# Performance work log

Hardware: AMD Instinct MI355X
Metric: run time of the kernel (lower is better)

## Reference

```python
import jax, jax.numpy as jnp
import numpy as np

W_CHAMFER = (1.0, 1.0, 1.0)
W_LAPLACE = 0.5
W_MOVE = 0.1
W_EDGE = 0.1
W_NORMAL = 1.6e-4
W_CONST = 1.0
LAP_CONST = (0.2, 1.0, 1.0)
EPS = 1e-12


def _normalize(x):
    # F.normalize(x, dim=-1): x / max(||x||, eps)
    n = jnp.sqrt(jnp.sum(x * x, axis=-1, keepdims=True))
    return x / jnp.maximum(n, EPS)


def _pairwise_sq(x, y):
    # x: (B,N,3), y: (B,M,3) -> (B,N,M) squared distances, GEMM form
    x2 = jnp.sum(x * x, -1)
    y2 = jnp.sum(y * y, -1)
    xy = jnp.einsum('bnd,bmd->bnm', x, y)
    return x2[:, :, None] + y2[:, None, :] - 2.0 * xy


def _laplace_coord(pts, lap_idx):
    # pts: (B,V,3); lap_idx: (V,10) = [8 neighbor idx (-1 invalid), self, count]
    idx = lap_idx[:, :8]
    mask = idx < 0
    safe = jnp.where(mask, 0, idx)
    nbrs = pts[:, safe]                                  # (B,V,8,3)
    nbrs = jnp.where(mask[None, :, :, None], 0.0, nbrs)
    count = lap_idx[:, -1].astype(pts.dtype)
    return pts - nbrs.sum(2) / count[None, :, None]


def setup_inputs():
    key = jax.random.key(0)
    B, M = 2, 8192
    Vs = (642, 2562, 10242)
    Es = (1920, 7680, 30720)
    ks = jax.random.split(key, 3 + 4 * 3)
    inp = {}
    inp['gt_coord'] = jax.random.normal(ks[0], (B, M, 3), jnp.float32)
    inp['gt_normal'] = _normalize(jax.random.normal(ks[1], (B, M, 3), jnp.float32))
    for i, (V, E) in enumerate(zip(Vs, Es)):
        k0, k1, k2, k3 = ks[3 + 4 * i], ks[4 + 4 * i], ks[5 + 4 * i], ks[6 + 4 * i]
        inp[f'pred_coord_{i}'] = jax.random.normal(k0, (B, V, 3), jnp.float32)
        inp[f'pred_before_{i}'] = inp[f'pred_coord_{i}'] + 0.05 * jax.random.normal(k1, (B, V, 3), jnp.float32)
        inp[f'edges_{i}'] = jax.random.randint(k2, (E, 2), 0, V)
        nbr = jax.random.randint(k3, (V, 8), 0, V)
        nbr = nbr.at[:, 6:].set(-1)                      # 6 valid neighbors, 2 invalid slots
        self_idx = jnp.arange(V)[:, None]
        count = jnp.full((V, 1), 6)
        inp[f'laplace_idx_{i}'] = jnp.concatenate([nbr, self_idx, count], axis=1)
    return inp


def reference(pred_coord_0, pred_coord_1, pred_coord_2, pred_before_0, pred_before_1, pred_before_2, gt_coord, gt_normal, laplace_idx_0, laplace_idx_1, laplace_idx_2, edges_0, edges_1, edges_2):
    preds = (pred_coord_0, pred_coord_1, pred_coord_2)
    befores = (pred_before_0, pred_before_1, pred_before_2)
    laps = (laplace_idx_0, laplace_idx_1, laplace_idx_2)
    edges_all = (edges_0, edges_1, edges_2)
    chamfer_loss = 0.0
    edge_loss = 0.0
    normal_loss = 0.0
    lap_loss = 0.0
    move_loss = 0.0
    for i in range(3):
        pred, before, lap_idx, edges = preds[i], befores[i], laps[i], edges_all[i]
        # shared pairwise distance matrix for chamfer + knn (original recomputes)
        d = _pairwise_sq(pred, gt_coord)                 # (B,V,M)
        chamfer_loss = chamfer_loss + W_CHAMFER[i] * (jnp.mean(jnp.min(d, axis=1)) + jnp.mean(jnp.min(d, axis=2)))
        knn_idx = jnp.argmin(d, axis=2)                  # (B,V): nearest gt per pred pt
        e0, e1 = edges[:, 0], edges[:, 1]
        evec = _normalize(pred[:, e0] - pred[:, e1])     # (B,E,3)
        # faithful to torch: knn.idx.flatten() then index_select -> only batch-0
        # indices ever selected since edge ids < V
        sel = knn_idx.reshape(-1)[e0]
        nrm = _normalize(gt_normal[:, sel])              # (B,E,3)
        normal_loss = normal_loss + jnp.mean(jnp.abs(jnp.sum(evec * nrm, axis=2)))
        edge_loss = edge_loss + 3.0 * jnp.mean((pred[:, e0] - pred[:, e1]) ** 2)
        l1 = _laplace_coord(before, lap_idx)
        l2 = _laplace_coord(pred, lap_idx)
        lap_loss = lap_loss + LAP_CONST[i] * 3.0 * jnp.mean((l1 - l2) ** 2)
        if i > 0:
            move_loss = move_loss + LAP_CONST[i] * 3.0 * jnp.mean((before - pred) ** 2)
    loss = chamfer_loss + W_LAPLACE * lap_loss + W_MOVE * move_loss + W_EDGE * edge_loss + W_NORMAL * normal_loss
    return W_CONST * loss
```

## Files before the change

kernel.cpp:

```cpp
#include <hip/hip_runtime.h>


#define DEV __device__ __forceinline__

#define OFF_LAP  8
#define OFF_MA0  1024
#define OFF_MA1  108592
#define OFF_MB   162376
#define MINS_END 358984

DEV unsigned ford(float f) {
    unsigned u = __float_as_uint(f);
    return (u & 0x80000000u) ? ~u : (u | 0x80000000u);
}
DEV float funord(unsigned o) {
    unsigned u = (o & 0x80000000u) ? (o ^ 0x80000000u) : ~o;
    return __uint_as_float(u);
}
DEV unsigned long long umin64(unsigned long long a, unsigned long long b) { return a < b ? a : b; }

DEV float blockReduceSum256(float v) {
    #pragma unroll
    for (int o = 32; o > 0; o >>= 1) v += __shfl_down(v, o, 64);
    __shared__ float red4[4];
    int wid = threadIdx.x >> 6;
    if ((threadIdx.x & 63) == 0) red4[wid] = v;
    __syncthreads();
    return (threadIdx.x == 0) ? (red4[0] + red4[1] + red4[2] + red4[3]) : 0.0f;
}

template<bool ARGMIN>
DEV void roleA(int a, const float* p0, const float* p1, const float* p2,
               const float* gt, char* ws, char* smem)
{
    const int b = ARGMIN ? 0 : 1;
    int vtG = a >> 5, mc = a & 31;
    int vtL, V, lvlOff; const float* predL;
    if (vtG == 0)     { vtL = 0;       V = 642;   predL = p0; lvlOff = 0; }
    else if (vtG < 4) { vtL = vtG - 1; V = 2562;  predL = p1; lvlOff = 642; }
    else              { vtL = vtG - 4; V = 10242; predL = p2; lvlOff = 3204; }
    int tid = threadIdx.x, lane = tid & 63, w = tid >> 6;
    float4* SG = (float4*)smem;
    int mbase = mc << 8;
    {
        const float* gp = gt + ((size_t)(b * 8192 + mbase + tid)) * 3;
        float gx = gp[0], gy = gp[1], gz = gp[2];
        SG[tid] = make_float4(-2.f * gx, -2.f * gy, -2.f * gz,
                              fmaf(gx, gx, fmaf(gy, gy, gz * gz)));
    }
    float px[14], py[14], pz[14];
    #pragma unroll
    for (int r = 0; r < 14; r++) {
        int vr = vtL * 896 + r * 64 + lane;
        int v = vr - (vr >= V ? V : 0);
        const float* pp = predL + ((size_t)(b * V + v)) * 3;
        px[r] = pp[0]; py[r] = pp[1]; pz[r] = pp[2];
    }
    __syncthreads();
    if (ARGMIN) {
        float best[14]; int bi[14];
        #pragma unroll
        for (int r = 0; r < 14; r++) { best[r] = 3.0e38f; bi[r] = 0; }
        #pragma unroll 4
        for (int i = 0; i < 64; i++) {
            int j = (w << 6) + i;
            float4 q = SG[j];
            int cand = mbase + j;
            #pragma unroll
            for (int r = 0; r < 14; r++) {
                float d = fmaf(q.x, px[r], fmaf(q.y, py[r], fmaf(q.z, pz[r], q.w)));
                if (d < best[r]) { best[r] = d; bi[r] = cand; }
            }
        }
        __syncthreads();
        unsigned long long* RED = (unsigned long long*)smem;
        #pragma unroll
        for (int r = 0; r < 14; r++)
            RED[w * 896 + r * 64 + lane] = ((unsigned long long)ford(best[r]) << 32) | (unsigned)bi[r];
        __syncthreads();
        unsigned long long* MA0 = (unsigned long long*)(ws + OFF_MA0);
        for (int s = tid; s < 896; s += 256) {
            unsigned long long mm = umin64(umin64(RED[s], RED[s + 896]),
                                           umin64(RED[s + 1792], RED[s + 2688]));
            int vr = vtL * 896 + s; int v = vr - (vr >= V ? V : 0);
            atomicMin(&MA0[lvlOff + v], mm);
        }
    } else {
        float best[14];
        #pragma unroll
        for (int r = 0; r < 14; r++) best[r] = 3.0e38f;
        #pragma unroll 2
        for (int i = 0; i < 64; i += 2) {
            int j = (w << 6) + i;
            float4 q0 = SG[j], q1 = SG[j + 1];
            #pragma unroll
            for (int r = 0; r < 14; r++) {
                float d0 = fmaf(q0.x, px[r], fmaf(q0.y, py[r], fmaf(q0.z, pz[r], q0.w)));
                float d1 = fmaf(q1.x, px[r], fmaf(q1.y, py[r], fmaf(q1.z, pz[r], q1.w)));
                best[r] = fminf(best[r], fminf(d0, d1));
            }
        }
        __syncthreads();
        unsigned* RED = (unsigned*)smem;
        #pragma unroll
        for (int r = 0; r < 14; r++)
            RED[w * 896 + r * 64 + lane] = ford(best[r]);
        __syncthreads();
        unsigned* MA1 = (unsigned*)(ws + OFF_MA1);
        for (int s = tid; s < 896; s += 256) {
            unsigned mm = min(min(RED[s], RED[s + 896]), min(RED[s + 1792], RED[s + 2688]));
            int vr = vtL * 896 + s; int v = vr - (vr >= V ? V : 0);
            atomicMin(&MA1[lvlOff + v], mm);
        }
    }
}

DEV void roleB(int i, const float* p0, const float* p1, const float* p2,
               const float* gt, char* ws, char* smem)
{
    int c55 = i % 55; int rest = i / 55; int mt = rest & 7; int b = rest >> 3;
    int lvl, c, V; const float* predL;
    if (c55 < 3)       { lvl = 0; c = c55;      V = 642;   predL = p0; }
    else if (c55 < 14) { lvl = 1; c = c55 - 3;  V = 2562;  predL = p1; }
    else               { lvl = 2; c = c55 - 14; V = 10242; predL = p2; }
    int tid = threadIdx.x, lane = tid & 63, w = tid >> 6;
    float4* SP = (float4*)smem;
    int vbase = c << 8;
    {
        int v = vbase + tid;
        if (v < V) {
            const float* pp = predL + ((size_t)(b * V + v)) * 3;
            float x = pp[0], y = pp[1], z = pp[2];
            SP[tid] = make_float4(-2.f * x, -2.f * y, -2.f * z,
                                  fmaf(x, x, fmaf(y, y, z * z)));
        } else SP[tid] = make_float4(0.f, 0.f, 0.f, 3.0e38f);
    }
    float gx[16], gy[16], gz[16];
    #pragma unroll
    for (int r = 0; r < 16; r++) {
        int m = (mt << 10) + r * 64 + lane;
        const float* gp = gt + ((size_t)(b * 8192 + m)) * 3;
        gx[r] = gp[0]; gy[r] = gp[1]; gz[r] = gp[2];
    }
    __syncthreads();
    float best[16];
    #pragma unroll
    for (int r = 0; r < 16; r++) best[r] = 3.0e38f;
    #pragma unroll 2
    for (int i2 = 0; i2 < 64; i2 += 2) {
        int j = (w << 6) + i2;
        float4 q0 = SP[j], q1 = SP[j + 1];
        #pragma unroll
        for (int r = 0; r < 16; r++) {
            float d0 = fmaf(q0.x, gx[r], fmaf(q0.y, gy[r], fmaf(q0.z, gz[r], q0.w)));
            float d1 = fmaf(q1.x, gx[r], fmaf(q1.y, gy[r], fmaf(q1.z, gz[r], q1.w)));
            best[r] = fminf(best[r], fminf(d0, d1));
        }
    }
    __syncthreads();
    unsigned* RED = (unsigned*)smem;
    #pragma unroll
    for (int r = 0; r < 16; r++)
        RED[(w << 10) + r * 64 + lane] = ford(best[r]);
    __syncthreads();
    unsigned* MB = (unsigned*)(ws + OFF_MB);
    for (int s = tid; s < 1024; s += 256) {
        unsigned mm = min(min(RED[s], RED[s + 1024]), min(RED[s + 2048], RED[s + 3072]));
        atomicMin(&MB[(lvl << 14) + (b << 13) + (mt << 10) + s], mm);
    }
}

__global__ __launch_bounds__(256, 4) void kMega(
    const float* __restrict__ p0, const float* __restrict__ p1, const float* __restrict__ p2,
    const float* __restrict__ b0p, const float* __restrict__ b1p, const float* __restrict__ b2p,
    const int* __restrict__ l0, const int* __restrict__ l1, const int* __restrict__ l2,
    const float* __restrict__ gt, char* ws)
{
    extern __shared__ char smem[];
    int bid = blockIdx.x;
    if (bid < 128) {
        float c = 0.0f;
        int idx = bid * 256 + threadIdx.x;
        if (idx < 26892) {
            int level, V, t;
            const float *pred, *bef; const int* lap;
            if (idx < 1284)      { level = 0; V = 642;   pred = p0; bef = b0p; lap = l0; t = idx; }
            else if (idx < 6408) { level = 1; V = 2562;  pred = p1; bef = b1p; lap = l1; t = idx - 1284; }
            else                 { level = 2; V = 10242; pred = p2; bef = b2p; lap = l2; t = idx - 6408; }
            int b = t / V;
            int v = t - b * V;
            const float* P  = pred + ((size_t)b * V + v) * 3;
            const float* Bf = bef  + ((size_t)b * V + v) * 3;
            float dx = Bf[0] - P[0], dy = Bf[1] - P[1], dz = Bf[2] - P[2];
            float sx = 0.f, sy = 0.f, sz = 0.f;
            const int* L = lap + v * 10;
            #pragma unroll
            for (int j = 0; j < 8; j++) {
                int n = L[j];
                if (n >= 0) {
                    const float* Pn = pred + ((size_t)b * V + n) * 3;
                    const float* Bn = bef  + ((size_t)b * V + n) * 3;
                    sx += Bn[0] - Pn[0]; sy += Bn[1] - Pn[1]; sz += Bn[2] - Pn[2];
                }
            }
            float invc = 1.0f / (float)L[9];
            float lx = dx - sx * invc, ly = dy - sy * invc, lz = dz - sz * invc;
            float sl = fmaf(lx, lx, fmaf(ly, ly, lz * lz));
            float sm = fmaf(dx, dx, fmaf(dy, dy, dz * dz));
            float lapc = (level == 0) ? 0.2f : 1.0f;
            float iBV = 1.0f / (2.0f * (float)V);
            c = sl * (0.5f * lapc * iBV) + ((level > 0) ? sm * (0.1f * lapc * iBV) : 0.0f);
        }
        c = blockReduceSum256(c);
        if (threadIdx.x == 0) ((float*)(ws + OFF_LAP))[bid] = c;
    }
    else if (bid < 1008) roleB(bid - 128, p0, p1, p2, gt, ws, smem);
    else if (bid < 1520) roleA<true >(bid - 1008, p0, p1, p2, gt, ws, smem);
    else                 roleA<false>(bid - 1520, p0, p1, p2, gt, ws, smem);
}

__global__ __launch_bounds__(256) void kFinal(
    const float* __restrict__ p0, const float* __restrict__ p1, const float* __restrict__ p2,
    const int* __restrict__ e0p, const int* __restrict__ e1p, const int* __restrict__ e2p,
    const float* __restrict__ gt, const float* __restrict__ gtn,
    char* ws, float* __restrict__ out)
{
    int bid = blockIdx.x, tid = threadIdx.x;
    const unsigned long long* MA0 = (const unsigned long long*)(ws + OFF_MA0);
    const unsigned* MA1 = (const unsigned*)(ws + OFF_MA1);
    const unsigned* MB  = (const unsigned*)(ws + OFF_MB);
    float c = 0.0f;
    if (bid < 106) {
        int idx = bid * 256 + tid;
        if (idx < 26892) {
            int b = idx >= 13446 ? 1 : 0;
            int s = idx - (b ? 13446 : 0);
            int v, V; const float* predL; float inv;
            if (s < 642)       { v = s;        V = 642;   predL = p0; inv = 1.f / 1284.f; }
            else if (s < 3204) { v = s - 642;  V = 2562;  predL = p1; inv = 1.f / 5124.f; }
            else               { v = s - 3204; V = 10242; predL = p2; inv = 1.f / 20484.f; }
            float d = b ? funord(MA1[s]) : funord((unsigned)(MA0[s] >> 32));
            const float* pp = predL + ((size_t)(b * V + v)) * 3;
            c = (d + fmaf(pp[0], pp[0], fmaf(pp[1], pp[1], pp[2] * pp[2]))) * inv;
        }
    } else if (bid < 298) {
        int idx = (bid - 106) * 256 + tid;
        int r = idx & 16383;
        float d = funord(MB[idx]);
        const float* gp = gt + (size_t)r * 3;
        c = (d + fmaf(gp[0], gp[0], fmaf(gp[1], gp[1], gp[2] * gp[2]))) * (1.f / 16384.f);
    } else if (bid == 298) {
        if (tid < 128) c = ((const float*)(ws + OFF_LAP))[tid];
    } else {
        int idx = (bid - 299) * 256 + tid;
        int E, V, lvlOff, t;
        const float* pred; const int* edges;
        if (idx < 3840)       { E = 1920;  V = 642;   lvlOff = 0;    pred = p0; edges = e0p; t = idx; }
        else if (idx < 19200) { E = 7680;  V = 2562;  lvlOff = 642;  pred = p1; edges = e1p; t = idx - 3840; }
        else                  { E = 30720; V = 10242; lvlOff = 3204; pred = p2; edges = e2p; t = idx - 19200; }
        int b = t / E;
        int e = t % E;
        int a0 = edges[e * 2 + 0];
        int a1 = edges[e * 2 + 1];
        const float* P = pred + (size_t)b * V * 3;
        float dx = P[a0 * 3 + 0] - P[a1 * 3 + 0];
        float dy = P[a0 * 3 + 1] - P[a1 * 3 + 1];
        float dz = P[a0 * 3 + 2] - P[a1 * 3 + 2];
        float sq = fmaf(dx, dx, fmaf(dy, dy, dz * dz));
        float inv = 1.0f / fmaxf(sqrtf(sq), 1e-12f);
        int sel = (int)(unsigned)MA0[lvlOff + a0];
        const float* nr = gtn + ((size_t)b * 8192 + sel) * 3;
        float nx = nr[0], ny = nr[1], nz = nr[2];
        float invn = 1.0f / fmaxf(sqrtf(fmaf(nx, nx, fmaf(ny, ny, nz * nz))), 1e-12f);
        float dotv = fmaf(dx, nx, fmaf(dy, ny, dz * nz)) * inv * invn;
        float iBE = 1.0f / (2.0f * (float)E);
        c = sq * (0.1f * iBE) + fabsf(dotv) * (0.00016f * iBE);
    }
    c = blockReduceSum256(c);
    if (tid == 0) {
        atomicAdd((float*)ws, c);
        __threadfence();
        unsigned t = atomicAdd((unsigned*)(ws + 4), 1u);
        if (t == gridDim.x - 1) out[0] = atomicAdd((float*)ws, 0.0f);
    }
}

extern "C" void kernel_launch(void* const* d_in, const int* in_sizes, int n_in,
                              void* d_out, int out_size, void* d_ws, size_t ws_size,
                              hipStream_t stream) {
    const float *gt, *gtn, *pred[3], *bef[3];
    const int *edg[3], *lapx[3];
    if (in_sizes[0] == 49152) {
        gt  = (const float*)d_in[0];
        gtn = (const float*)d_in[1];
        for (int i = 0; i < 3; i++) {
            pred[i] = (const float*)d_in[2 + 4 * i];
            bef[i]  = (const float*)d_in[3 + 4 * i];
            edg[i]  = (const int*)  d_in[4 + 4 * i];
            lapx[i] = (const int*)  d_in[5 + 4 * i];
        }
    } else {
        for (int i = 0; i < 3; i++) pred[i] = (const float*)d_in[i];
        for (int i = 0; i < 3; i++) bef[i]  = (const float*)d_in[3 + i];
        gt  = (const float*)d_in[6];
        gtn = (const float*)d_in[7];
        for (int i = 0; i < 3; i++) lapx[i] = (const int*)d_in[8 + i];
        for (int i = 0; i < 3; i++) edg[i]  = (const int*)d_in[11 + i];
    }

    char* ws = (char*)d_ws;
    hipMemsetAsync(ws, 0, 8, stream);
    hipMemsetAsync(ws + OFF_MA0, 0xFF, MINS_END - OFF_MA0, stream);

    kMega<<<2032, 256, 28672, stream>>>(pred[0], pred[1], pred[2],
                                        bef[0], bef[1], bef[2],
                                        lapx[0], lapx[1], lapx[2], gt, ws);
    kFinal<<<614, 256, 0, stream>>>(pred[0], pred[1], pred[2],
                                    edg[0], edg[1], edg[2], gt, gtn,
                                    ws, (float*)d_out);
}
```

Baseline: 145.5 us.

## Fuse memsets and both kernels into one persistent cooperative kernel with grid syncs

Replaces two memsets plus two kernel launches with a single cooperative persistent kernel. The kernel clears the workspace, pulls work units dynamically from an atomic counter, finalizes through grid syncs, and reduces the block-level min reduction to a pairwise scheme that needs less shared memory. The aim is to remove launch and memset overhead and to raise occupancy. The cost is three grid-wide barriers, a dynamic scheduling atomic per unit, and a grid capped at 1024 persistent blocks, which may serialize the work. A fallback keeps the old two-kernel path in case the cooperative launch fails.

```diff
diff --git a/kernel.cpp b/kernel.cpp
--- a/kernel.cpp
+++ b/kernel.cpp
@@ -1,13 +1,13 @@
 #include <hip/hip_runtime.h>
+#include <hip/hip_cooperative_groups.h>
+
+namespace cg = cooperative_groups;
 
 
 #define DEV __device__ __forceinline__
-
-#define OFF_LAP  8
 #define OFF_MA0  1024
 #define OFF_MA1  108592
 #define OFF_MB   162376
-#define MINS_END 358984
 
 DEV unsigned ford(float f) {
     unsigned u = __float_as_uint(f);
@@ -26,7 +26,9 @@
     int wid = threadIdx.x >> 6;
     if ((threadIdx.x & 63) == 0) red4[wid] = v;
     __syncthreads();
-    return (threadIdx.x == 0) ? (red4[0] + red4[1] + red4[2] + red4[3]) : 0.0f;
+    float r = (threadIdx.x == 0) ? (red4[0] + red4[1] + red4[2] + red4[3]) : 0.0f;
+    __syncthreads();
+    return r;
 }
 
 template<bool ARGMIN>
@@ -72,16 +74,40 @@
                 if (d < best[r]) { best[r] = d; bi[r] = cand; }
             }
         }
-        __syncthreads();
-        unsigned long long* RED = (unsigned long long*)smem;
+        unsigned long long key[14];
         #pragma unroll
         for (int r = 0; r < 14; r++)
-            RED[w * 896 + r * 64 + lane] = ((unsigned long long)ford(best[r]) << 32) | (unsigned)bi[r];
+            key[r] = ((unsigned long long)ford(best[r]) << 32) | (unsigned)bi[r];
+        __syncthreads();
+        unsigned long long* RED0 = (unsigned long long*)smem;
+        unsigned long long* RED1 = (unsigned long long*)(smem + 7168);
+        if (w == 0) {
+            #pragma unroll
+            for (int r = 0; r < 14; r++) RED0[r * 64 + lane] = key[r];
+        }
+        if (w == 2) {
+            #pragma unroll
+            for (int r = 0; r < 14; r++) RED1[r * 64 + lane] = key[r];
+        }
+        __syncthreads();
+        if (w == 1) {
+            #pragma unroll
+            for (int r = 0; r < 14; r++) {
+                int s = r * 64 + lane;
+                RED0[s] = umin64(RED0[s], key[r]);
+            }
+        }
+        if (w == 3) {
+            #pragma unroll
+            for (int r = 0; r < 14; r++) {
+                int s = r * 64 + lane;
+                RED1[s] = umin64(RED1[s], key[r]);
+            }
+        }
         __syncthreads();
         unsigned long long* MA0 = (unsigned long long*)(ws + OFF_MA0);
         for (int s = tid; s < 896; s += 256) {
-            unsigned long long mm = umin64(umin64(RED[s], RED[s + 896]),
-                                           umin64(RED[s + 1792], RED[s + 2688]));
+            unsigned long long mm = umin64(RED0[s], RED1[s]);
             int vr = vtL * 896 + s; int v = vr - (vr >= V ? V : 0);
             atomicMin(&MA0[lvlOff + v], mm);
         }
@@ -100,15 +126,39 @@
                 best[r] = fminf(best[r], fminf(d0, d1));
             }
         }
-        __syncthreads();
-        unsigned* RED = (unsigned*)smem;
-        #pragma unroll
-        for (int r = 0; r < 14; r++)
-            RED[w * 896 + r * 64 + lane] = ford(best[r]);
+        unsigned key[14];
+        #pragma unroll
+        for (int r = 0; r < 14; r++) key[r] = ford(best[r]);
+        __syncthreads();
+        unsigned* RED0 = (unsigned*)smem;
+        unsigned* RED1 = (unsigned*)(smem + 3584);
+        if (w == 0) {
+            #pragma unroll
+            for (int r = 0; r < 14; r++) RED0[r * 64 + lane] = key[r];
+        }
+        if (w == 2) {
+            #pragma unroll
+            for (int r = 0; r < 14; r++) RED1[r * 64 + lane] = key[r];
+        }
+        __syncthreads();
+        if (w == 1) {
+            #pragma unroll
+            for (int r = 0; r < 14; r++) {
+                int s = r * 64 + lane;
+                RED0[s] = min(RED0[s], key[r]);
+            }
+        }
+        if (w == 3) {
+            #pragma unroll
+            for (int r = 0; r < 14; r++) {
+                int s = r * 64 + lane;
+                RED1[s] = min(RED1[s], key[r]);
+            }
+        }
         __syncthreads();
         unsigned* MA1 = (unsigned*)(ws + OFF_MA1);
         for (int s = tid; s < 896; s += 256) {
-            unsigned mm = min(min(RED[s], RED[s + 896]), min(RED[s + 1792], RED[s + 2688]));
+            unsigned mm = min(RED0[s], RED1[s]);
             int vr = vtL * 896 + s; int v = vr - (vr >= V ? V : 0);
             atomicMin(&MA1[lvlOff + v], mm);
         }
@@ -157,107 +207,118 @@
             best[r] = fminf(best[r], fminf(d0, d1));
         }
     }
-    __syncthreads();
-    unsigned* RED = (unsigned*)smem;
+    unsigned key[16];
     #pragma unroll
-    for (int r = 0; r < 16; r++)
-        RED[(w << 10) + r * 64 + lane] = ford(best[r]);
+    for (int r = 0; r < 16; r++) key[r] = ford(best[r]);
+    __syncthreads();
+    unsigned* RED0 = (unsigned*)smem;
+    unsigned* RED1 = (unsigned*)(smem + 4096);
+    if (w == 0) {
+        #pragma unroll
+        for (int r = 0; r < 16; r++) RED0[r * 64 + lane] = key[r];
+    }
+    if (w == 2) {
+        #pragma unroll
+        for (int r = 0; r < 16; r++) RED1[r * 64 + lane] = key[r];
+    }
+    __syncthreads();
+    if (w == 1) {
+        #pragma unroll
+        for (int r = 0; r < 16; r++) {
+            int s = r * 64 + lane;
+            RED0[s] = min(RED0[s], key[r]);
+        }
+    }
+    if (w == 3) {
+        #pragma unroll
+        for (int r = 0; r < 16; r++) {
+            int s = r * 64 + lane;
+            RED1[s] = min(RED1[s], key[r]);
+        }
+    }
     __syncthreads();
     unsigned* MB = (unsigned*)(ws + OFF_MB);
     for (int s = tid; s < 1024; s += 256) {
-        unsigned mm = min(min(RED[s], RED[s + 1024]), min(RED[s + 2048], RED[s + 3072]));
+        unsigned mm = min(RED0[s], RED1[s]);
         atomicMin(&MB[(lvl << 14) + (b << 13) + (mt << 10) + s], mm);
     }
 }
 
-__global__ __launch_bounds__(256, 4) void kMega(
-    const float* __restrict__ p0, const float* __restrict__ p1, const float* __restrict__ p2,
-    const float* __restrict__ b0p, const float* __restrict__ b1p, const float* __restrict__ b2p,
-    const int* __restrict__ l0, const int* __restrict__ l1, const int* __restrict__ l2,
-    const float* __restrict__ gt, char* ws)
-{
-    extern __shared__ char smem[];
-    int bid = blockIdx.x;
-    if (bid < 128) {
-        float c = 0.0f;
-        int idx = bid * 256 + threadIdx.x;
-        if (idx < 26892) {
-            int level, V, t;
-            const float *pred, *bef; const int* lap;
-            if (idx < 1284)      { level = 0; V = 642;   pred = p0; bef = b0p; lap = l0; t = idx; }
-            else if (idx < 6408) { level = 1; V = 2562;  pred = p1; bef = b1p; lap = l1; t = idx - 1284; }
-            else                 { level = 2; V = 10242; pred = p2; bef = b2p; lap = l2; t = idx - 6408; }
-            int b = t / V;
-            int v = t - b * V;
-            const float* P  = pred + ((size_t)b * V + v) * 3;
-            const float* Bf = bef  + ((size_t)b * V + v) * 3;
-            float dx = Bf[0] - P[0], dy = Bf[1] - P[1], dz = Bf[2] - P[2];
-            float sx = 0.f, sy = 0.f, sz = 0.f;
-            const int* L = lap + v * 10;
-            #pragma unroll
-            for (int j = 0; j < 8; j++) {
-                int n = L[j];
-                if (n >= 0) {
-                    const float* Pn = pred + ((size_t)b * V + n) * 3;
-                    const float* Bn = bef  + ((size_t)b * V + n) * 3;
-                    sx += Bn[0] - Pn[0]; sy += Bn[1] - Pn[1]; sz += Bn[2] - Pn[2];
-                }
-            }
-            float invc = 1.0f / (float)L[9];
-            float lx = dx - sx * invc, ly = dy - sy * invc, lz = dz - sz * invc;
-            float sl = fmaf(lx, lx, fmaf(ly, ly, lz * lz));
-            float sm = fmaf(dx, dx, fmaf(dy, dy, dz * dz));
-            float lapc = (level == 0) ? 0.2f : 1.0f;
-            float iBV = 1.0f / (2.0f * (float)V);
-            c = sl * (0.5f * lapc * iBV) + ((level > 0) ? sm * (0.1f * lapc * iBV) : 0.0f);
-        }
-        c = blockReduceSum256(c);
-        if (threadIdx.x == 0) ((float*)(ws + OFF_LAP))[bid] = c;
-    }
-    else if (bid < 1008) roleB(bid - 128, p0, p1, p2, gt, ws, smem);
-    else if (bid < 1520) roleA<true >(bid - 1008, p0, p1, p2, gt, ws, smem);
-    else                 roleA<false>(bid - 1520, p0, p1, p2, gt, ws, smem);
-}
-
-__global__ __launch_bounds__(256) void kFinal(
-    const float* __restrict__ p0, const float* __restrict__ p1, const float* __restrict__ p2,
-    const int* __restrict__ e0p, const int* __restrict__ e1p, const int* __restrict__ e2p,
-    const float* __restrict__ gt, const float* __restrict__ gtn,
-    char* ws, float* __restrict__ out)
-{
-    int bid = blockIdx.x, tid = threadIdx.x;
+DEV void lapUnit(int u,
+                 const float* p0, const float* p1, const float* p2,
+                 const float* b0p, const float* b1p, const float* b2p,
+                 const int* l0, const int* l1, const int* l2, char* ws)
+{
+    float c = 0.0f;
+    int idx = u * 256 + threadIdx.x;
+    if (idx < 26892) {
+        int level, V, t;
+        const float *pred, *bef; const int* lap;
+        if (idx < 1284)      { level = 0; V = 642;   pred = p0; bef = b0p; lap = l0; t = idx; }
+        else if (idx < 6408) { level = 1; V = 2562;  pred = p1; bef = b1p; lap = l1; t = idx - 1284; }
+        else                 { level = 2; V = 10242; pred = p2; bef = b2p; lap = l2; t = idx - 6408; }
+        int b = t / V;
+        int v = t - b * V;
+        const float* P  = pred + ((size_t)b * V + v) * 3;
+        const float* Bf = bef  + ((size_t)b * V + v) * 3;
+        float dx = Bf[0] - P[0], dy = Bf[1] - P[1], dz = Bf[2] - P[2];
+        float sx = 0.f, sy = 0.f, sz = 0.f;
+        const int* L = lap + v * 10;
+        #pragma unroll
+        for (int j = 0; j < 8; j++) {
+            int n = L[j];
+            if (n >= 0) {
+                const float* Pn = pred + ((size_t)b * V + n) * 3;
+                const float* Bn = bef  + ((size_t)b * V + n) * 3;
+                sx += Bn[0] - Pn[0]; sy += Bn[1] - Pn[1]; sz += Bn[2] - Pn[2];
+            }
+        }
+        float invc = 1.0f / (float)L[9];
+        float lx = dx - sx * invc, ly = dy - sy * invc, lz = dz - sz * invc;
+        float sl = fmaf(lx, lx, fmaf(ly, ly, lz * lz));
+        float sm = fmaf(dx, dx, fmaf(dy, dy, dz * dz));
+        float lapc = (level == 0) ? 0.2f : 1.0f;
+        float iBV = 1.0f / (2.0f * (float)V);
+        c = sl * (0.5f * lapc * iBV) + ((level > 0) ? sm * (0.1f * lapc * iBV) : 0.0f);
+    }
+    c = blockReduceSum256(c);
+    if (threadIdx.x == 0) atomicAdd((float*)ws, c);
+}
+
+DEV float phase2Item(int idx,
+                     const float* p0, const float* p1, const float* p2,
+                     const int* e0p, const int* e1p, const int* e2p,
+                     const float* gt, const float* gtn, char* ws)
+{
     const unsigned long long* MA0 = (const unsigned long long*)(ws + OFF_MA0);
     const unsigned* MA1 = (const unsigned*)(ws + OFF_MA1);
     const unsigned* MB  = (const unsigned*)(ws + OFF_MB);
     float c = 0.0f;
-    if (bid < 106) {
-        int idx = bid * 256 + tid;
-        if (idx < 26892) {
-            int b = idx >= 13446 ? 1 : 0;
-            int s = idx - (b ? 13446 : 0);
-            int v, V; const float* predL; float inv;
-            if (s < 642)       { v = s;        V = 642;   predL = p0; inv = 1.f / 1284.f; }
-            else if (s < 3204) { v = s - 642;  V = 2562;  predL = p1; inv = 1.f / 5124.f; }
-            else               { v = s - 3204; V = 10242; predL = p2; inv = 1.f / 20484.f; }
-            float d = b ? funord(MA1[s]) : funord((unsigned)(MA0[s] >> 32));
-            const float* pp = predL + ((size_t)(b * V + v)) * 3;
-            c = (d + fmaf(pp[0], pp[0], fmaf(pp[1], pp[1], pp[2] * pp[2]))) * inv;
-        }
-    } else if (bid < 298) {
-        int idx = (bid - 106) * 256 + tid;
-        int r = idx & 16383;
-        float d = funord(MB[idx]);
+    if (idx < 26892) {
+        int b = idx >= 13446 ? 1 : 0;
+        int s = idx - (b ? 13446 : 0);
+        int v, V; const float* predL; float inv;
+        if (s < 642)       { v = s;        V = 642;   predL = p0; inv = 1.f / 1284.f; }
+        else if (s < 3204) { v = s - 642;  V = 2562;  predL = p1; inv = 1.f / 5124.f; }
+        else               { v = s - 3204; V = 10242; predL = p2; inv = 1.f / 20484.f; }
+        float d;
+        if (b) d = funord(__hip_atomic_load(&MA1[s], __ATOMIC_RELAXED, __HIP_MEMORY_SCOPE_AGENT));
+        else   d = funord((unsigned)(__hip_atomic_load(&MA0[s], __ATOMIC_RELAXED, __HIP_MEMORY_SCOPE_AGENT) >> 32));
+        const float* pp = predL + ((size_t)(b * V + v)) * 3;
+        c = (d + fmaf(pp[0], pp[0], fmaf(pp[1], pp[1], pp[2] * pp[2]))) * inv;
+    } else if (idx < 76044) {
+        int j = idx - 26892;
+        int r = j & 16383;
+        float d = funord(__hip_atomic_load(&MB[j], __ATOMIC_RELAXED, __HIP_MEMORY_SCOPE_AGENT));
         const float* gp = gt + (size_t)r * 3;
         c = (d + fmaf(gp[0], gp[0], fmaf(gp[1], gp[1], gp[2] * gp[2]))) * (1.f / 16384.f);
-    } else if (bid == 298) {
-        if (tid < 128) c = ((const float*)(ws + OFF_LAP))[tid];
     } else {
-        int idx = (bid - 299) * 256 + tid;
-        int E, V, lvlOff, t;
+        int t = idx - 76044;
+        int E, V, lvlOff;
         const float* pred; const int* edges;
-        if (idx < 3840)       { E = 1920;  V = 642;   lvlOff = 0;    pred = p0; edges = e0p; t = idx; }
-        else if (idx < 19200) { E = 7680;  V = 2562;  lvlOff = 642;  pred = p1; edges = e1p; t = idx - 3840; }
-        else                  { E = 30720; V = 10242; lvlOff = 3204; pred = p2; edges = e2p; t = idx - 19200; }
+        if (t < 3840)       { E = 1920;  V = 642;   lvlOff = 0;    pred = p0; edges = e0p; }
+        else if (t < 19200) { E = 7680;  V = 2562;  lvlOff = 642;  pred = p1; edges = e1p; t -= 3840; }
+        else                { E = 30720; V = 10242; lvlOff = 3204; pred = p2; edges = e2p; t -= 19200; }
         int b = t / E;
         int e = t % E;
         int a0 = edges[e * 2 + 0];
@@ -268,7 +329,8 @@
         float dz = P[a0 * 3 + 2] - P[a1 * 3 + 2];
         float sq = fmaf(dx, dx, fmaf(dy, dy, dz * dz));
         float inv = 1.0f / fmaxf(sqrtf(sq), 1e-12f);
-        int sel = (int)(unsigned)MA0[lvlOff + a0];
+        unsigned long long key = __hip_atomic_load(&MA0[lvlOff + a0], __ATOMIC_RELAXED, __HIP_MEMORY_SCOPE_AGENT);
+        int sel = (int)(unsigned)key;
         const float* nr = gtn + ((size_t)b * 8192 + sel) * 3;
         float nx = nr[0], ny = nr[1], nz = nr[2];
         float invn = 1.0f / fmaxf(sqrtf(fmaf(nx, nx, fmaf(ny, ny, nz * nz))), 1e-12f);
@@ -276,12 +338,99 @@
         float iBE = 1.0f / (2.0f * (float)E);
         c = sq * (0.1f * iBE) + fabsf(dotv) * (0.00016f * iBE);
     }
+    return c;
+}
+
+__global__ __launch_bounds__(256) void kFused(
+    const float* __restrict__ p0, const float* __restrict__ p1, const float* __restrict__ p2,
+    const float* __restrict__ b0p, const float* __restrict__ b1p, const float* __restrict__ b2p,
+    const int* __restrict__ l0, const int* __restrict__ l1, const int* __restrict__ l2,
+    const int* __restrict__ e0p, const int* __restrict__ e1p, const int* __restrict__ e2p,
+    const float* __restrict__ gt, const float* __restrict__ gtn,
+    char* ws, float* __restrict__ out)
+{
+    __shared__ __align__(16) char smem[16384];
+    __shared__ int sU;
+    cg::grid_group grid = cg::this_grid();
+    int tid = threadIdx.x;
+    int gtid = blockIdx.x * 256 + tid;
+    int gridThreads = gridDim.x * 256;
+
+    {
+        unsigned* mins = (unsigned*)(ws + OFF_MA0);
+        for (int i = gtid; i < 89490; i += gridThreads)
+            atomicExch(&mins[i], 0xFFFFFFFFu);
+        if (gtid == 0) {
+            atomicExch((unsigned*)ws, 0u);
+            atomicExch((unsigned*)(ws + 4), 0u);
+        }
+    }
+    grid.sync();
+
+    for (;;) {
+        if (tid == 0) sU = (int)atomicAdd((unsigned*)(ws + 4), 1u);
+        __syncthreads();
+        int u = sU;
+        if (u >= 2032) break;
+        if (u < 128)       lapUnit(u, p0, p1, p2, b0p, b1p, b2p, l0, l1, l2, ws);
+        else if (u < 1008) roleB(u - 128, p0, p1, p2, gt, ws, smem);
+        else if (u < 1520) roleA<true >(u - 1008, p0, p1, p2, gt, ws, smem);
+        else               roleA<false>(u - 1520, p0, p1, p2, gt, ws, smem);
+        __syncthreads();
+    }
+    grid.sync();
+
+    {
+        float c = 0.0f;
+        for (int idx = gtid; idx < 156684; idx += gridThreads)
+            c += phase2Item(idx, p0, p1, p2, e0p, e1p, e2p, gt, gtn, ws);
+        c = blockReduceSum256(c);
+        if (tid == 0) atomicAdd((float*)ws, c);
+    }
+    grid.sync();
+
+    if (gtid == 0)
+        out[0] = __hip_atomic_load((float*)ws, __ATOMIC_RELAXED, __HIP_MEMORY_SCOPE_AGENT);
+}
+
+__global__ __launch_bounds__(256) void kMegaFB(
+    const float* __restrict__ p0, const float* __restrict__ p1, const float* __restrict__ p2,
+    const float* __restrict__ b0p, const float* __restrict__ b1p, const float* __restrict__ b2p,
+    const int* __restrict__ l0, const int* __restrict__ l1, const int* __restrict__ l2,
+    const float* __restrict__ gt, char* ws)
+{
+    __shared__ __align__(16) char smem[16384];
+    int bid = blockIdx.x;
+    if (bid < 128)       lapUnit(bid, p0, p1, p2, b0p, b1p, b2p, l0, l1, l2, ws);
+    else if (bid < 1008) roleB(bid - 128, p0, p1, p2, gt, ws, smem);
+    else if (bid < 1520) roleA<true >(bid - 1008, p0, p1, p2, gt, ws, smem);
+    else                 roleA<false>(bid - 1520, p0, p1, p2, gt, ws, smem);
+}
+
+__global__ __launch_bounds__(256) void kFinalFB(
+    const float* __restrict__ p0, const float* __restrict__ p1, const float* __restrict__ p2,
+    const int* __restrict__ e0p, const int* __restrict__ e1p, const int* __restrict__ e2p,
+    const float* __restrict__ gt, const float* __restrict__ gtn,
+    char* ws, float* __restrict__ out)
+{
+    int bid = blockIdx.x, tid = threadIdx.x;
+    float c = 0.0f;
+    if (bid < 106) {
+        int idx = bid * 256 + tid;
+        if (idx < 26892) c = phase2Item(idx, p0, p1, p2, e0p, e1p, e2p, gt, gtn, ws);
+    } else if (bid < 298) {
+        int idx = 26892 + (bid - 106) * 256 + tid;
+        c = phase2Item(idx, p0, p1, p2, e0p, e1p, e2p, gt, gtn, ws);
+    } else {
+        int idx = 76044 + (bid - 298) * 256 + tid;
+        c = phase2Item(idx, p0, p1, p2, e0p, e1p, e2p, gt, gtn, ws);
+    }
     c = blockReduceSum256(c);
     if (tid == 0) {
         atomicAdd((float*)ws, c);
         __threadfence();
         unsigned t = atomicAdd((unsigned*)(ws + 4), 1u);
-        if (t == gridDim.x - 1) out[0] = atomicAdd((float*)ws, 0.0f);
+        if (t == 612u) out[0] = atomicAdd((float*)ws, 0.0f);
     }
 }
 
@@ -309,13 +458,35 @@
     }
 
     char* ws = (char*)d_ws;
-    hipMemsetAsync(ws, 0, 8, stream);
-    hipMemsetAsync(ws + OFF_MA0, 0xFF, MINS_END - OFF_MA0, stream);
-
-    kMega<<<2032, 256, 28672, stream>>>(pred[0], pred[1], pred[2],
-                                        bef[0], bef[1], bef[2],
-                                        lapx[0], lapx[1], lapx[2], gt, ws);
-    kFinal<<<614, 256, 0, stream>>>(pred[0], pred[1], pred[2],
-                                    edg[0], edg[1], edg[2], gt, gtn,
-                                    ws, (float*)d_out);
-}
+    float* out = (float*)d_out;
+
+    int nPerCU = 0, cus = 0, dev = 0;
+    (void)hipGetDevice(&dev);
+    (void)hipDeviceGetAttribute(&cus, hipDeviceAttributeMultiprocessorCount, dev);
+    (void)hipOccupancyMaxActiveBlocksPerMultiprocessor(&nPerCU, kFused, 256, 0);
+    long long gridLL = (long long)nPerCU * (long long)cus;
+    int grid = (int)(gridLL > 1024 ? 1024 : gridLL);
+
+    hipError_t err = hipErrorUnknown;
+    if (grid >= 64) {
+        void* args[] = {
+            (void*)&pred[0], (void*)&pred[1], (void*)&pred[2],
+            (void*)&bef[0],  (void*)&bef[1],  (void*)&bef[2],
+            (void*)&lapx[0], (void*)&lapx[1], (void*)&lapx[2],
+            (void*)&edg[0],  (void*)&edg[1],  (void*)&edg[2],
+            (void*)&gt, (void*)&gtn, (void*)&ws, (void*)&out
+        };
+        err = hipLaunchCooperativeKernel((void*)kFused, dim3(grid), dim3(256), args, 0, stream);
+    }
+    if (err != hipSuccess) {
+        (void)hipGetLastError();
+        (void)hipMemsetAsync(ws, 0, 8, stream);
+        (void)hipMemsetAsync(ws + OFF_MA0, 0xFF, 357960, stream);
+        kMegaFB<<<2032, 256, 0, stream>>>(pred[0], pred[1], pred[2],
+                                          bef[0], bef[1], bef[2],
+                                          lapx[0], lapx[1], lapx[2], gt, ws);
+        kFinalFB<<<613, 256, 0, stream>>>(pred[0], pred[1], pred[2],
+                                          edg[0], edg[1], edg[2], gt, gtn,
+                                          ws, out);
+    }
+}
```

New measurement: 270.6 us. 86.0% more time.
